# Kernel optimization log

Measured on AMD Instinct MI355X. Metric: run time of the kernel, lower is better.

The kernel has to match this reference:

```python
import jax, jax.numpy as jnp
import numpy as np

B = 4096
D = 68 * 68  # 4624
L = 68
E = 1024


def setup_inputs() -> dict:
    key = jax.random.key(0)
    ks = jax.random.split(key, 24)
    rn = lambda k, shape, scale: jax.random.normal(k, shape, dtype=jnp.float32) * scale
    inp = {
        "x": rn(ks[0], (B, D), 1.0),
        "eps": rn(ks[1], (B, L), 1.0),
        # weights scaled ~1/sqrt(fan_in) to avoid sigmoid saturation
        "fc11_w": rn(ks[2], (E, D), 1.0 / np.sqrt(D)),
        "fc11_b": rn(ks[3], (E,), 0.01),
        "fc12_w": rn(ks[4], (E, D), 1.0 / np.sqrt(D)),
        "fc12_b": rn(ks[5], (E,), 0.01),
        "fc21_w": rn(ks[6], (L, E), 1.0 / np.sqrt(E)),
        "fc21_b": rn(ks[7], (L,), 0.01),
        "fc22_w": rn(ks[8], (L, E), 1.0 / np.sqrt(E)),
        "fc22_b": rn(ks[9], (L,), 0.01),
        "W3": rn(ks[10], (5, L, L), 1.0 / np.sqrt(L)),
        "b3": rn(ks[11], (5, L), 0.01),
        "W4": rn(ks[12], (5, L, L), 1.0 / np.sqrt(L)),
        "b4": rn(ks[13], (5, L), 0.01),
        "W5": rn(ks[14], (3, L, L), 1.0 / np.sqrt(L)),
        "b5": rn(ks[15], (3, L), 0.01),
        "fc6_w": rn(ks[16], (D, D), 1.0 / np.sqrt(D)),
        "fc6_b": rn(ks[17], (D,), 0.01),
        "fcy_w": rn(ks[18], (1, L), 1.0 / np.sqrt(L)),
        "fcy_b": rn(ks[19], (1,), 0.01),
    }
    return inp


def _forward(x, eps, fc11_w, fc11_b, fc12_w, fc12_b, fc21_w, fc21_b,
             fc22_w, fc22_b, W3, b3, W4, b4, W5, b5, fc6_w, fc6_b, fcy_w, fcy_b):
    b = x.shape[0]
    # encode (dropout in eval mode -> identity)
    h11 = jax.nn.relu(x @ fc11_w.T + fc11_b)
    h12 = jax.nn.relu(x @ fc12_w.T + fc12_b)
    mu = h11 @ fc21_w.T + fc21_b          # [B, 68]
    logvar = h12 @ fc22_w.T + fc22_b      # [B, 68]
    # reparameterize
    z = mu + eps * jnp.exp(0.5 * logvar)
    y = mu @ fcy_w.T + fcy_b              # [B, 1]
    # decode: 5 parallel 68-dim branches (vectorized over branch axis k)
    h3 = jnp.einsum('bd,kod->kbo', z, W3) + b3[:, None, :]     # [5,B,68]
    # source: h31 has no sigmoid, h32..h35 do
    h3 = jnp.concatenate([h3[:1], jax.nn.sigmoid(h3[1:])], axis=0)
    h4 = jax.nn.sigmoid(jnp.einsum('kbd,kod->kbo', h3, W4) + b4[:, None, :])
    # source reuses fc53 for branches 4 and 5: weight index map [0,1,2,2,2]
    idx = jnp.array([0, 1, 2, 2, 2])
    h5 = jnp.einsum('kbd,kod->kbo', h4, W5[idx]) + b5[idx][:, None, :]  # [5,B,68]
    # source: h6 = h51 only (other branch outer-products are dead code)
    h51 = h5[0]                                                # [B,68]
    outer = (h51[:, :, None] * h51[:, None, :]).reshape(b, D)  # bmm outer product
    recon = jax.nn.sigmoid(outer @ fc6_w.T + fc6_b)            # [B, 4624]
    return recon, mu, logvar, y


def reference(x, eps, fc11_w, fc11_b, fc12_w, fc12_b, fc21_w, fc21_b,
              fc22_w, fc22_b, W3, b3, W4, b4, W5, b5, fc6_w, fc6_b, fcy_w, fcy_b):
    return _forward(x, eps, fc11_w, fc11_b, fc12_w, fc12_b, fc21_w, fc21_b,
                    fc22_w, fc22_b, W3, b3, W4, b4, W5, b5, fc6_w, fc6_b, fcy_w, fcy_b)
```

## Files before the change

### kernel.cpp

```cpp
#include <hip/hip_runtime.h>
#include <hip/hip_bf16.h>
#include <cstdint>
#include <cstddef>

typedef __bf16 bf16x8 __attribute__((ext_vector_type(8)));
typedef __bf16 bf16x4 __attribute__((ext_vector_type(4)));
typedef float  floatx4 __attribute__((ext_vector_type(4)));

#define DEV __device__ __forceinline__

DEV __bf16 f2b(float x) { return (__bf16)x; }

DEV void async_ld16(const void* g, void* l) {
    __builtin_amdgcn_global_load_lds(
        (const __attribute__((address_space(1))) unsigned int*)g,
        (__attribute__((address_space(3))) unsigned int*)l,
        16, 0, 0);
}

#define BATCH 4096
#define DDIM  4624
#define DPAD  4672
#define LDIM  68
#define EDIM  1024
#define N1    2048
#define KB    2048
#define N2PAD 4736
#define NPAIR 2346
#define K2PAD 2368

__global__ void cvt_pad(const float* __restrict__ src, int rows_valid, int K,
                        __bf16* __restrict__ dst, int rows_total) {
    const int gpr = DPAD / 4;
    const long total = (long)rows_total * gpr;
    for (long g = blockIdx.x * (long)blockDim.x + threadIdx.x; g < total;
         g += gridDim.x * (long)blockDim.x) {
        int row = (int)(g / gpr);
        int c4  = (int)(g - (long)row * gpr) * 4;
        bf16x4 v;
        if (row < rows_valid && c4 < K) {
            floatx4 f = *(const floatx4*)(src + (size_t)row * K + c4);
            v[0] = f2b(f[0]); v[1] = f2b(f[1]); v[2] = f2b(f[2]); v[3] = f2b(f[3]);
        } else {
            v[0] = v[1] = v[2] = v[3] = (__bf16)0.0f;
        }
        *(bf16x4*)(dst + (size_t)row * DPAD + c4) = v;
    }
}

__global__ void pad_w2(const float* __restrict__ w21, const float* __restrict__ w22,
                       __bf16* __restrict__ dst) {
    const int total = 144 * 512;
    for (int g = blockIdx.x * blockDim.x + threadIdx.x; g < total;
         g += gridDim.x * blockDim.x) {
        int row = g >> 9;
        int c4  = (g & 511) * 4;
        bf16x4 v;
        v[0] = v[1] = v[2] = v[3] = (__bf16)0.0f;
        if (row < 68 && c4 < 1024) {
            floatx4 f = *(const floatx4*)(w21 + (size_t)row * EDIM + c4);
            v[0] = f2b(f[0]); v[1] = f2b(f[1]); v[2] = f2b(f[2]); v[3] = f2b(f[3]);
        } else if (row >= 68 && row < 136 && c4 >= 1024) {
            floatx4 f = *(const floatx4*)(w22 + (size_t)(row - 68) * EDIM + (c4 - 1024));
            v[0] = f2b(f[0]); v[1] = f2b(f[1]); v[2] = f2b(f[2]); v[3] = f2b(f[3]);
        }
        *(bf16x4*)(dst + (size_t)row * KB + c4) = v;
    }
}

DEV void build_ptab(unsigned short* ptab, int t, int nthr) {
    for (int i = t; i < LDIM; i += nthr) {
        int p0 = i * (137 - i) / 2;
        for (int j = i; j < LDIM; ++j)
            ptab[p0 + (j - i)] = (unsigned short)((i << 8) | j);
    }
}

__global__ void w6sym_build(const float* __restrict__ w6, __bf16* __restrict__ dst) {
    __shared__ float row[DDIM];
    __shared__ unsigned short ptab[K2PAD];
    const int o = blockIdx.x;
    const int t = threadIdx.x;
    if (o < DDIM) {
        const float* src = w6 + (size_t)o * DDIM;
        for (int idx = t; idx < DDIM / 4; idx += 256)
            *(floatx4*)(row + idx * 4) = *(const floatx4*)(src + idx * 4);
    }
    build_ptab(ptab, t, 256);
    __syncthreads();
    for (int p4 = t; p4 < K2PAD / 4; p4 += 256) {
        bf16x4 v;
#pragma unroll
        for (int u = 0; u < 4; ++u) {
            int p = p4 * 4 + u;
            float val = 0.f;
            if (o < DDIM && p < NPAIR) {
                int ij = ptab[p];
                int i = ij >> 8, j = ij & 255;
                val = (i == j) ? row[i * LDIM + i] : (row[i * LDIM + j] + row[j * LDIM + i]);
            }
            v[u] = f2b(val);
        }
        *(bf16x4*)(dst + (size_t)o * K2PAD + p4 * 4) = v;
    }
}

template <int EPI>
__launch_bounds__(256, 2)
__global__ void gemm_bt(const __bf16* __restrict__ A, int lda,
                        const __bf16* __restrict__ W, int ldb, int KT,
                        __bf16* __restrict__ outb, float* __restrict__ outf, int ldc,
                        const float* __restrict__ bias0, const float* __restrict__ bias1) {
    __shared__ __align__(16) __bf16 smA[128 * 64];
    __shared__ __align__(16) __bf16 smB[128 * 64];

    const int t  = threadIdx.x;
    const int l  = t & 63;
    const int w  = t >> 6;
    const int m0 = blockIdx.x * 128;
    const int n0 = blockIdx.y * 128;
    const int wm = (w & 1) * 64;
    const int wn = (w >> 1) * 64;

    const int srow   = t >> 3;
    const int schunk = (t & 7) ^ (srow & 7);
    const __bf16* pa = A + (size_t)(m0 + srow) * lda + schunk * 8;
    const __bf16* pb = W + (size_t)(n0 + srow) * ldb + schunk * 8;
    char* dA = (char*)smA + t * 16;
    char* dB = (char*)smB + t * 16;

    floatx4 acc[4][4];
#pragma unroll
    for (int mi = 0; mi < 4; ++mi)
#pragma unroll
        for (int ni = 0; ni < 4; ++ni) {
            floatx4 z = {0.f, 0.f, 0.f, 0.f};
            acc[mi][ni] = z;
        }

    for (int kt = 0; kt < KT; ++kt) {
#pragma unroll
        for (int i = 0; i < 4; ++i) {
            async_ld16(pa + (size_t)i * 32 * lda, dA + i * 4096);
            async_ld16(pb + (size_t)i * 32 * ldb, dB + i * 4096);
        }
        pa += 64; pb += 64;
        __syncthreads();

#pragma unroll
        for (int h = 0; h < 2; ++h) {
            bf16x8 af[4], bfr[4];
#pragma unroll
            for (int mi = 0; mi < 4; ++mi) {
                int r = wm + mi * 16 + (l & 15);
                int c = ((h << 2) | (l >> 4)) ^ (r & 7);
                af[mi] = *(const bf16x8*)((const char*)smA + r * 128 + c * 16);
            }
#pragma unroll
            for (int ni = 0; ni < 4; ++ni) {
                int r = wn + ni * 16 + (l & 15);
                int c = ((h << 2) | (l >> 4)) ^ (r & 7);
                bfr[ni] = *(const bf16x8*)((const char*)smB + r * 128 + c * 16);
            }
#pragma unroll
            for (int mi = 0; mi < 4; ++mi)
#pragma unroll
                for (int ni = 0; ni < 4; ++ni)
                    acc[mi][ni] = __builtin_amdgcn_mfma_f32_16x16x32_bf16(af[mi], bfr[ni],
                                                                         acc[mi][ni], 0, 0, 0);
        }
        __syncthreads();
    }

    const int colbase = n0 + wn + (l & 15);
    const int rowbase = m0 + wm + (l >> 4) * 4;
#pragma unroll
    for (int ni = 0; ni < 4; ++ni) {
        int col = colbase + ni * 16;
        if (EPI == 1 && col >= DDIM) continue;
        float bias = (EPI == 0)
                         ? ((col < 1024) ? bias0[col] : bias1[col - 1024])
                         : bias0[col];
#pragma unroll
        for (int mi = 0; mi < 4; ++mi) {
            int row = rowbase + mi * 16;
#pragma unroll
            for (int r = 0; r < 4; ++r) {
                float v = acc[mi][ni][r] + bias;
                if (EPI == 0) {
                    v = v > 0.f ? v : 0.f;
                    outb[(size_t)(row + r) * ldc + col] = f2b(v);
                } else {
                    v = 1.f / (1.f + __expf(-v));
                    outf[(size_t)(row + r) * ldc + col] = v;
                }
            }
        }
    }
}

__launch_bounds__(64, 4)
__global__ void gemmB(const __bf16* __restrict__ h, const __bf16* __restrict__ w2,
                      float* __restrict__ muvar) {
    const int l    = threadIdx.x;
    const int m0   = blockIdx.x * 16;
    const int k0   = blockIdx.y * 512;
    const int row  = l & 15;
    const int quad = l >> 4;

    floatx4 acc[9];
#pragma unroll
    for (int ni = 0; ni < 9; ++ni) {
        floatx4 z = {0.f, 0.f, 0.f, 0.f};
        acc[ni] = z;
    }

    const __bf16* ap = h + (size_t)(m0 + row) * KB + k0 + quad * 8;
    for (int kt = 0; kt < 16; ++kt) {
        bf16x8 a = *(const bf16x8*)ap;
        ap += 32;
#pragma unroll
        for (int ni = 0; ni < 9; ++ni) {
            const __bf16* bp = w2 + (size_t)(ni * 16 + row) * KB + k0 + kt * 32 + quad * 8;
            bf16x8 b = *(const bf16x8*)bp;
            acc[ni] = __builtin_amdgcn_mfma_f32_16x16x32_bf16(a, b, acc[ni], 0, 0, 0);
        }
    }
#pragma unroll
    for (int ni = 0; ni < 9; ++ni) {
        int col = ni * 16 + row;
        if (col < 136) {
#pragma unroll
            for (int r = 0; r < 4; ++r) {
                int orow = m0 + quad * 4 + r;
                atomicAdd(&muvar[(size_t)orow * 136 + col], acc[ni][r]);
            }
        }
    }
}

__global__ void decode(const float* __restrict__ muvar, const float* __restrict__ eps,
                       const float* __restrict__ b21, const float* __restrict__ b22,
                       const float* __restrict__ W3, const float* __restrict__ b3,
                       const float* __restrict__ W4, const float* __restrict__ b4,
                       const float* __restrict__ W5, const float* __restrict__ b5,
                       const float* __restrict__ fcyw, const float* __restrict__ fcyb,
                       float* __restrict__ out_mu, float* __restrict__ out_lv,
                       float* __restrict__ out_y, __bf16* __restrict__ A2) {
    __shared__ float w3s[DDIM], w4s[DDIM], w5s[DDIM];
    __shared__ float b3s[LDIM], b4s[LDIM], b5s[LDIM], fys[LDIM];
    __shared__ float zb[16][LDIM], h3b[16][LDIM], h51b[16][LDIM];
    __shared__ unsigned short ptab[K2PAD];

    const int t  = threadIdx.x;
    const int r0 = blockIdx.x * 16;

    for (int i = t; i < DDIM; i += 256) {
        w3s[i] = W3[i];
        w4s[i] = W4[i];
        w5s[i] = W5[i];
    }
    if (t < LDIM) {
        b3s[t] = b3[t];
        b4s[t] = b4[t];
        b5s[t] = b5[t];
        fys[t] = fcyw[t];
    }
    build_ptab(ptab, t, 256);
    __syncthreads();

    for (int idx = t; idx < 16 * LDIM; idx += 256) {
        int r = idx / LDIM, o = idx - r * LDIM;
        int row = r0 + r;
        float mu = muvar[(size_t)row * 136 + o] + b21[o];
        float lv = muvar[(size_t)row * 136 + 68 + o] + b22[o];
        float z  = mu + eps[(size_t)row * LDIM + o] * __expf(0.5f * lv);
        zb[r][o] = z;
        out_mu[(size_t)row * LDIM + o] = mu;
        out_lv[(size_t)row * LDIM + o] = lv;
    }
    if (t < 16) {
        int row = r0 + t;
        float s = fcyb[0];
        for (int o = 0; o < LDIM; ++o)
            s += (muvar[(size_t)row * 136 + o] + b21[o]) * fys[o];
        out_y[row] = s;
    }
    __syncthreads();

    for (int idx = t; idx < 16 * LDIM; idx += 256) {
        int r = idx / LDIM, o = idx - r * LDIM;
        float s = b3s[o];
        for (int d = 0; d < LDIM; ++d) s += zb[r][d] * w3s[o * LDIM + d];
        h3b[r][o] = s;
    }
    __syncthreads();

    for (int idx = t; idx < 16 * LDIM; idx += 256) {
        int r = idx / LDIM, o = idx - r * LDIM;
        float s = b4s[o];
        for (int d = 0; d < LDIM; ++d) s += h3b[r][d] * w4s[o * LDIM + d];
        zb[r][o] = 1.f / (1.f + __expf(-s));
    }
    __syncthreads();

    for (int idx = t; idx < 16 * LDIM; idx += 256) {
        int r = idx / LDIM, o = idx - r * LDIM;
        float s = b5s[o];
        for (int d = 0; d < LDIM; ++d) s += zb[r][d] * w5s[o * LDIM + d];
        h51b[r][o] = s;
    }
    __syncthreads();

    for (int idx = t; idx < 16 * (K2PAD / 4); idx += 256) {
        int r  = idx / (K2PAD / 4);
        int p4 = (idx - r * (K2PAD / 4)) * 4;
        int row = r0 + r;
        bf16x4 v;
#pragma unroll
        for (int u = 0; u < 4; ++u) {
            int p = p4 + u;
            float val = 0.f;
            if (p < NPAIR) {
                int ij = ptab[p];
                val = h51b[r][ij >> 8] * h51b[r][ij & 255];
            }
            v[u] = f2b(val);
        }
        *(bf16x4*)(A2 + (size_t)row * K2PAD + p4) = v;
    }
}

extern "C" void kernel_launch(void* const* d_in, const int* in_sizes, int n_in,
                              void* d_out, int out_size, void* d_ws, size_t ws_size,
                              hipStream_t stream) {
    const float* x    = (const float*)d_in[0];
    const float* eps  = (const float*)d_in[1];
    const float* w11  = (const float*)d_in[2];
    const float* b11  = (const float*)d_in[3];
    const float* w12  = (const float*)d_in[4];
    const float* b12  = (const float*)d_in[5];
    const float* w21  = (const float*)d_in[6];
    const float* b21  = (const float*)d_in[7];
    const float* w22  = (const float*)d_in[8];
    const float* b22  = (const float*)d_in[9];
    const float* W3   = (const float*)d_in[10];
    const float* b3   = (const float*)d_in[11];
    const float* W4   = (const float*)d_in[12];
    const float* b4   = (const float*)d_in[13];
    const float* W5   = (const float*)d_in[14];
    const float* b5   = (const float*)d_in[15];
    const float* w6   = (const float*)d_in[16];
    const float* b6   = (const float*)d_in[17];
    const float* fcyw = (const float*)d_in[18];
    const float* fcyb = (const float*)d_in[19];

    float* out       = (float*)d_out;
    float* out_recon = out;
    float* out_mu    = out + (size_t)BATCH * DDIM;
    float* out_lv    = out_mu + (size_t)BATCH * LDIM;
    float* out_y     = out_lv + (size_t)BATCH * LDIM;

    char* ws = (char*)d_ws;
    size_t off = 0;
    __bf16* xb     = (__bf16*)(ws + off); off += (size_t)BATCH * DPAD * 2;
    __bf16* w1_pad = (__bf16*)(ws + off); off += (size_t)N1 * DPAD * 2;
    __bf16* w6s    = (__bf16*)(ws + off); off += (size_t)N2PAD * K2PAD * 2;
    __bf16* hbuf   = (__bf16*)(ws + off); off += (size_t)BATCH * KB * 2;
    __bf16* w2_pad = (__bf16*)(ws + off); off += (size_t)144 * KB * 2;
    float*  muvar  = (float*) (ws + off); off += (size_t)BATCH * 136 * 4;
    __bf16* A2     = (__bf16*)(ws + off);

    hipMemsetAsync(muvar, 0, (size_t)BATCH * 136 * 4, stream);

    cvt_pad<<<2048, 256, 0, stream>>>(x, BATCH, DDIM, xb, BATCH);
    cvt_pad<<<512, 256, 0, stream>>>(w11, 1024, DDIM, w1_pad, 1024);
    cvt_pad<<<512, 256, 0, stream>>>(w12, 1024, DDIM, w1_pad + (size_t)1024 * DPAD, 1024);
    w6sym_build<<<N2PAD, 256, 0, stream>>>(w6, w6s);
    pad_w2<<<72, 256, 0, stream>>>(w21, w22, w2_pad);

    gemm_bt<0><<<dim3(32, 16), 256, 0, stream>>>(
        xb, DPAD, w1_pad, DPAD, DPAD / 64, hbuf, nullptr, N1, b11, b12);

    gemmB<<<dim3(BATCH / 16, 4), 64, 0, stream>>>(hbuf, w2_pad, muvar);

    decode<<<BATCH / 16, 256, 0, stream>>>(muvar, eps, b21, b22, W3, b3, W4, b4, W5, b5,
                                           fcyw, fcyb, out_mu, out_lv, out_y, A2);

    gemm_bt<1><<<dim3(32, N2PAD / 128), 256, 0, stream>>>(
        A2, K2PAD, w6s, K2PAD, K2PAD / 64, nullptr, out_recon, DDIM, b6, nullptr);
}
```

Before: 533.1 us.

## Fuse prep kernels, swizzle GEMM block order, replace atomics with split-K partials

Merges the five conversion/padding/symmetrization kernels into one launch that dispatches on block index, removing several launch gaps. Both bt GEMMs now use a 1D grid with an XCD-aware swizzle of block IDs so neighbouring tiles land on the same chiplet for L2 reuse. gemmB writes four split-K partial buffers instead of doing atomicAdd into a memset buffer, and decode sums the partials, which drops the memset and the atomics. The cost is extra workspace and extra reads in decode.

```diff
diff --git a/kernel.cpp b/kernel.cpp
--- a/kernel.cpp
+++ b/kernel.cpp
@@ -28,45 +28,7 @@
 #define N2PAD 4736
 #define NPAIR 2346
 #define K2PAD 2368
-
-__global__ void cvt_pad(const float* __restrict__ src, int rows_valid, int K,
-                        __bf16* __restrict__ dst, int rows_total) {
-    const int gpr = DPAD / 4;
-    const long total = (long)rows_total * gpr;
-    for (long g = blockIdx.x * (long)blockDim.x + threadIdx.x; g < total;
-         g += gridDim.x * (long)blockDim.x) {
-        int row = (int)(g / gpr);
-        int c4  = (int)(g - (long)row * gpr) * 4;
-        bf16x4 v;
-        if (row < rows_valid && c4 < K) {
-            floatx4 f = *(const floatx4*)(src + (size_t)row * K + c4);
-            v[0] = f2b(f[0]); v[1] = f2b(f[1]); v[2] = f2b(f[2]); v[3] = f2b(f[3]);
-        } else {
-            v[0] = v[1] = v[2] = v[3] = (__bf16)0.0f;
-        }
-        *(bf16x4*)(dst + (size_t)row * DPAD + c4) = v;
-    }
-}
-
-__global__ void pad_w2(const float* __restrict__ w21, const float* __restrict__ w22,
-                       __bf16* __restrict__ dst) {
-    const int total = 144 * 512;
-    for (int g = blockIdx.x * blockDim.x + threadIdx.x; g < total;
-         g += gridDim.x * blockDim.x) {
-        int row = g >> 9;
-        int c4  = (g & 511) * 4;
-        bf16x4 v;
-        v[0] = v[1] = v[2] = v[3] = (__bf16)0.0f;
-        if (row < 68 && c4 < 1024) {
-            floatx4 f = *(const floatx4*)(w21 + (size_t)row * EDIM + c4);
-            v[0] = f2b(f[0]); v[1] = f2b(f[1]); v[2] = f2b(f[2]); v[3] = f2b(f[3]);
-        } else if (row >= 68 && row < 136 && c4 >= 1024) {
-            floatx4 f = *(const floatx4*)(w22 + (size_t)(row - 68) * EDIM + (c4 - 1024));
-            v[0] = f2b(f[0]); v[1] = f2b(f[1]); v[2] = f2b(f[2]); v[3] = f2b(f[3]);
-        }
-        *(bf16x4*)(dst + (size_t)row * KB + c4) = v;
-    }
-}
+#define NBX   32
 
 DEV void build_ptab(unsigned short* ptab, int t, int nthr) {
     for (int i = t; i < LDIM; i += nthr) {
@@ -76,32 +38,81 @@
     }
 }
 
-__global__ void w6sym_build(const float* __restrict__ w6, __bf16* __restrict__ dst) {
-    __shared__ float row[DDIM];
+#define PREP_GRID 7880
+__global__ __launch_bounds__(256) void prep(
+        const float* __restrict__ x, const float* __restrict__ w11,
+        const float* __restrict__ w12, const float* __restrict__ w21,
+        const float* __restrict__ w22, const float* __restrict__ w6,
+        __bf16* __restrict__ xb, __bf16* __restrict__ w1_pad,
+        __bf16* __restrict__ w2_pad, __bf16* __restrict__ w6s) {
+    __shared__ float rowbuf[DDIM];
     __shared__ unsigned short ptab[K2PAD];
-    const int o = blockIdx.x;
+    const int b = blockIdx.x;
     const int t = threadIdx.x;
-    if (o < DDIM) {
-        const float* src = w6 + (size_t)o * DDIM;
-        for (int idx = t; idx < DDIM / 4; idx += 256)
-            *(floatx4*)(row + idx * 4) = *(const floatx4*)(src + idx * 4);
-    }
-    build_ptab(ptab, t, 256);
-    __syncthreads();
-    for (int p4 = t; p4 < K2PAD / 4; p4 += 256) {
-        bf16x4 v;
-#pragma unroll
-        for (int u = 0; u < 4; ++u) {
-            int p = p4 * 4 + u;
-            float val = 0.f;
-            if (o < DDIM && p < NPAIR) {
-                int ij = ptab[p];
-                int i = ij >> 8, j = ij & 255;
-                val = (i == j) ? row[i * LDIM + i] : (row[i * LDIM + j] + row[j * LDIM + i]);
-            }
-            v[u] = f2b(val);
-        }
-        *(bf16x4*)(dst + (size_t)o * K2PAD + p4 * 4) = v;
+
+    if (b < 3072) {
+        const float* src;
+        __bf16* dst;
+        int rows, lb, vg;
+        if (b < 2048)      { src = x;   dst = xb;                          rows = BATCH; lb = b;        vg = 2048; }
+        else if (b < 2560) { src = w11; dst = w1_pad;                      rows = 1024;  lb = b - 2048; vg = 512; }
+        else               { src = w12; dst = w1_pad + (size_t)1024 * DPAD; rows = 1024; lb = b - 2560; vg = 512; }
+        const int gpr = DPAD / 4;
+        const long total = (long)rows * gpr;
+        for (long g = lb * 256L + t; g < total; g += vg * 256L) {
+            int row = (int)(g / gpr);
+            int c4  = (int)(g - (long)row * gpr) * 4;
+            bf16x4 v;
+            if (c4 < DDIM) {
+                floatx4 f = *(const floatx4*)(src + (size_t)row * DDIM + c4);
+                v[0] = f2b(f[0]); v[1] = f2b(f[1]); v[2] = f2b(f[2]); v[3] = f2b(f[3]);
+            } else {
+                v[0] = v[1] = v[2] = v[3] = (__bf16)0.0f;
+            }
+            *(bf16x4*)(dst + (size_t)row * DPAD + c4) = v;
+        }
+    } else if (b < 3144) {
+        const int lb = b - 3072;
+        const int total = 144 * 512;
+        for (int g = lb * 256 + t; g < total; g += 72 * 256) {
+            int row = g >> 9;
+            int c4  = (g & 511) * 4;
+            bf16x4 v;
+            v[0] = v[1] = v[2] = v[3] = (__bf16)0.0f;
+            if (row < 68 && c4 < 1024) {
+                floatx4 f = *(const floatx4*)(w21 + (size_t)row * EDIM + c4);
+                v[0] = f2b(f[0]); v[1] = f2b(f[1]); v[2] = f2b(f[2]); v[3] = f2b(f[3]);
+            } else if (row >= 68 && row < 136 && c4 >= 1024) {
+                floatx4 f = *(const floatx4*)(w22 + (size_t)(row - 68) * EDIM + (c4 - 1024));
+                v[0] = f2b(f[0]); v[1] = f2b(f[1]); v[2] = f2b(f[2]); v[3] = f2b(f[3]);
+            }
+            *(bf16x4*)(w2_pad + (size_t)row * KB + c4) = v;
+        }
+    } else {
+        const int o = b - 3144;
+        if (o < DDIM) {
+            const float* src = w6 + (size_t)o * DDIM;
+            for (int idx = t; idx < DDIM / 4; idx += 256)
+                *(floatx4*)(rowbuf + idx * 4) = *(const floatx4*)(src + idx * 4);
+        }
+        build_ptab(ptab, t, 256);
+        __syncthreads();
+        for (int p4 = t; p4 < K2PAD / 4; p4 += 256) {
+            bf16x4 v;
+#pragma unroll
+            for (int u = 0; u < 4; ++u) {
+                int p = p4 * 4 + u;
+                float val = 0.f;
+                if (o < DDIM && p < NPAIR) {
+                    int ij = ptab[p];
+                    int i = ij >> 8, j = ij & 255;
+                    val = (i == j) ? rowbuf[i * LDIM + i]
+                                   : (rowbuf[i * LDIM + j] + rowbuf[j * LDIM + i]);
+                }
+                v[u] = f2b(val);
+            }
+            *(bf16x4*)(w6s + (size_t)o * K2PAD + p4 * 4) = v;
+        }
     }
 }
 
@@ -117,8 +128,10 @@
     const int t  = threadIdx.x;
     const int l  = t & 63;
     const int w  = t >> 6;
-    const int m0 = blockIdx.x * 128;
-    const int n0 = blockIdx.y * 128;
+    const int cpx = gridDim.x >> 3;
+    const int swz = (blockIdx.x & 7) * cpx + (blockIdx.x >> 3);
+    const int m0  = (swz & (NBX - 1)) * 128;
+    const int n0  = (swz / NBX) * 128;
     const int wm = (w & 1) * 64;
     const int wn = (w >> 1) * 64;
 
@@ -207,6 +220,7 @@
     const int k0   = blockIdx.y * 512;
     const int row  = l & 15;
     const int quad = l >> 4;
+    float* mv = muvar + (size_t)blockIdx.y * BATCH * 136;
 
     floatx4 acc[9];
 #pragma unroll
@@ -233,7 +247,7 @@
 #pragma unroll
             for (int r = 0; r < 4; ++r) {
                 int orow = m0 + quad * 4 + r;
-                atomicAdd(&muvar[(size_t)orow * 136 + col], acc[ni][r]);
+                mv[(size_t)orow * 136 + col] = acc[ni][r];
             }
         }
     }
@@ -249,7 +263,7 @@
                        float* __restrict__ out_y, __bf16* __restrict__ A2) {
     __shared__ float w3s[DDIM], w4s[DDIM], w5s[DDIM];
     __shared__ float b3s[LDIM], b4s[LDIM], b5s[LDIM], fys[LDIM];
-    __shared__ float zb[16][LDIM], h3b[16][LDIM], h51b[16][LDIM];
+    __shared__ float zb[16][LDIM], h3b[16][LDIM], h51b[16][LDIM], mub[16][LDIM];
     __shared__ unsigned short ptab[K2PAD];
 
     const int t  = threadIdx.x;
@@ -272,21 +286,29 @@
     for (int idx = t; idx < 16 * LDIM; idx += 256) {
         int r = idx / LDIM, o = idx - r * LDIM;
         int row = r0 + r;
-        float mu = muvar[(size_t)row * 136 + o] + b21[o];
-        float lv = muvar[(size_t)row * 136 + 68 + o] + b22[o];
-        float z  = mu + eps[(size_t)row * LDIM + o] * __expf(0.5f * lv);
-        zb[r][o] = z;
+        float mu = b21[o];
+        float lv = b22[o];
+#pragma unroll
+        for (int s = 0; s < 4; ++s) {
+            const float* mv = muvar + (size_t)s * BATCH * 136 + (size_t)row * 136;
+            mu += mv[o];
+            lv += mv[68 + o];
+        }
+        float z = mu + eps[(size_t)row * LDIM + o] * __expf(0.5f * lv);
+        zb[r][o]  = z;
+        mub[r][o] = mu;
         out_mu[(size_t)row * LDIM + o] = mu;
         out_lv[(size_t)row * LDIM + o] = lv;
     }
+    __syncthreads();
+
     if (t < 16) {
         int row = r0 + t;
         float s = fcyb[0];
         for (int o = 0; o < LDIM; ++o)
-            s += (muvar[(size_t)row * 136 + o] + b21[o]) * fys[o];
+            s += mub[t][o] * fys[o];
         out_y[row] = s;
     }
-    __syncthreads();
 
     for (int idx = t; idx < 16 * LDIM; idx += 256) {
         int r = idx / LDIM, o = idx - r * LDIM;
@@ -368,18 +390,13 @@
     __bf16* w6s    = (__bf16*)(ws + off); off += (size_t)N2PAD * K2PAD * 2;
     __bf16* hbuf   = (__bf16*)(ws + off); off += (size_t)BATCH * KB * 2;
     __bf16* w2_pad = (__bf16*)(ws + off); off += (size_t)144 * KB * 2;
-    float*  muvar  = (float*) (ws + off); off += (size_t)BATCH * 136 * 4;
+    float*  muvar  = (float*) (ws + off); off += (size_t)4 * BATCH * 136 * 4;
     __bf16* A2     = (__bf16*)(ws + off);
 
-    hipMemsetAsync(muvar, 0, (size_t)BATCH * 136 * 4, stream);
-
-    cvt_pad<<<2048, 256, 0, stream>>>(x, BATCH, DDIM, xb, BATCH);
-    cvt_pad<<<512, 256, 0, stream>>>(w11, 1024, DDIM, w1_pad, 1024);
-    cvt_pad<<<512, 256, 0, stream>>>(w12, 1024, DDIM, w1_pad + (size_t)1024 * DPAD, 1024);
-    w6sym_build<<<N2PAD, 256, 0, stream>>>(w6, w6s);
-    pad_w2<<<72, 256, 0, stream>>>(w21, w22, w2_pad);
-
-    gemm_bt<0><<<dim3(32, 16), 256, 0, stream>>>(
+    prep<<<PREP_GRID, 256, 0, stream>>>(x, w11, w12, w21, w22, w6,
+                                        xb, w1_pad, w2_pad, w6s);
+
+    gemm_bt<0><<<(BATCH / 128) * (N1 / 128), 256, 0, stream>>>(
         xb, DPAD, w1_pad, DPAD, DPAD / 64, hbuf, nullptr, N1, b11, b12);
 
     gemmB<<<dim3(BATCH / 16, 4), 64, 0, stream>>>(hbuf, w2_pad, muvar);
@@ -387,6 +404,6 @@
     decode<<<BATCH / 16, 256, 0, stream>>>(muvar, eps, b21, b22, W3, b3, W4, b4, W5, b5,
                                            fcyw, fcyb, out_mu, out_lv, out_y, A2);
 
-    gemm_bt<1><<<dim3(32, N2PAD / 128), 256, 0, stream>>>(
+    gemm_bt<1><<<(BATCH / 128) * (N2PAD / 128), 256, 0, stream>>>(
         A2, K2PAD, w6s, K2PAD, K2PAD / 64, nullptr, out_recon, DDIM, b6, nullptr);
 }
```

Measured after the change: 537.9 us. About the same (+0.9%).
